# Optimization experiments

Measured on AMD Instinct MI355X. Metric: run time of the kernel, lower is better.

Reference implementation:

```python
import jax, jax.numpy as jnp
import numpy as np
import math

NH = 8      # n_heads
EPS = 1e-5  # LayerNorm eps (torch default)

def _pe(S, D):
    # Sin/cos positional encoding, faithful to PositionalEncoder
    pos = jnp.arange(S, dtype=jnp.float32)[:, None]
    div = jnp.exp(jnp.arange(0, D, 2, dtype=jnp.float32) * (-math.log(10000.0) / D))
    ang = pos * div  # (S, D/2)
    pe = jnp.zeros((S, D), jnp.float32)
    pe = pe.at[:, 0::2].set(jnp.sin(ang)).at[:, 1::2].set(jnp.cos(ang))
    return pe

def _ln(x, g, b):
    m = x.mean(-1, keepdims=True)
    v = ((x - m) ** 2).mean(-1, keepdims=True)
    return (x - m) / jnp.sqrt(v + EPS) * g + b

def setup_inputs() -> dict:
    key = jax.random.key(0)
    ks = jax.random.split(key, 6)
    S, H, W, D, dff = 512, 4, 4, 512, 2048
    x = jax.random.normal(ks[0], (S, H, W, D), jnp.float32)
    s = 1.0 / math.sqrt(D)
    Wq = jax.random.normal(ks[1], (D, D), jnp.float32) * s      # w_qs (used for q, k, v in sincos path)
    Wfc = jax.random.normal(ks[2], (D, D), jnp.float32) * s     # fc (no bias)
    W1 = jax.random.normal(ks[3], (dff, D), jnp.float32) * s    # ffn.w1
    b1 = jnp.zeros((dff,), jnp.float32)
    W2 = jax.random.normal(ks[4], (D, dff), jnp.float32) * (1.0 / math.sqrt(dff))  # ffn.w2
    b2 = jnp.zeros((D,), jnp.float32)
    g1 = jnp.ones((D,), jnp.float32); be1 = jnp.zeros((D,), jnp.float32)
    g2 = jnp.ones((D,), jnp.float32); be2 = jnp.zeros((D,), jnp.float32)
    return dict(x=x, Wq=Wq, Wfc=Wfc, W1=W1, b1=b1, W2=W2, b2=b2,
                g1=g1, be1=be1, g2=g2, be2=be2)

def reference(x, Wq, Wfc, W1, b1, W2, b2, g1, be1, g2, be2):
    S, H, Wd, D = x.shape
    depth = D // NH
    # sincos path: ALL of q,k,v use w_qs (source bug) and q==k==v since inputs are identical
    q = x @ Wq.T + _pe(S, D)[:, None, None, :]               # (S,H,W,D)
    # torch .view: raw memory reinterpretation (S,H,W,D) -> (H,W,S,NH,depth), then transpose(2,3)
    q5 = jnp.swapaxes(q.reshape(H, Wd, S, NH, depth), 2, 3)  # (H,W,NH,S,depth)
    k_t = jnp.swapaxes(q5, 3, 4)                             # (H,W,NH,depth,S)
    scale = 1.0 / math.sqrt(depth)
    # 'hwink,hwijm->hwinm': k and j are summed INDEPENDENTLY (rank-1 outer product of sums)
    bmm_qk = jnp.einsum('hwink,hwijm->hwinm', q5 * scale, k_t)   # (H,W,NH,S,S)
    qk = jax.nn.softmax(bmm_qk, axis=-1)
    qk = jnp.einsum('hwink,hwijm->hwinm', qk, k_t)               # second context pass
    attn_weights = jax.nn.softmax(qk, axis=-1)
    out = jnp.einsum('hwijk,hwikn->hwijn', attn_weights, q5)     # v == q5; (H,W,NH,S,depth)
    attn_out = out.reshape(S, H, Wd, NH * depth) @ Wfc.T         # raw reshape back, then fc
    o1 = _ln(x + attn_out, g1, be1)
    ffn = jax.nn.relu(o1 @ W1.T + b1) @ W2.T + b2
    return _ln(o1 + ffn, g2, be2)
```

## Files before the change

### kernel.cpp

```cpp
#include <hip/hip_runtime.h>
#include <hip/hip_bf16.h>
#include <math.h>


typedef short short8 __attribute__((ext_vector_type(8)));
typedef float f32x4 __attribute__((ext_vector_type(4)));

#define LN10K_OVER_256 0.03597789207803197f

__device__ __forceinline__ void gload16(const short* g, short* l) {
  __builtin_amdgcn_global_load_lds(
      (const __attribute__((address_space(1))) void*)g,
      (__attribute__((address_space(3))) void*)l, 16, 0, 0);
}

#define BAR() do { asm volatile("" ::: "memory"); \
                   __builtin_amdgcn_s_barrier();  \
                   asm volatile("" ::: "memory"); } while (0)

__device__ __forceinline__ short8 ldsfrag(const short* opbuf, int R, int fq) {
  int sr = R >> 1;
  int sp = (((R & 1) << 2) | fq) ^ (sr & 7);
  return *(const short8*)(opbuf + sr * 64 + sp * 8);
}

template<bool DOSTAGE, int WAITK>
__device__ __forceinline__ void tile_step(
    short* ldsb, int cur, int nx, int tt, int koff,
    const short* Ag0, const short* Ag1, const short* Bg0, const short* Bg1,
    int w, int fr, int fq, int wm, int wn, f32x4 (&acc)[8][4]) {
  const short* Abuf = ldsb + cur * 16384;
  const short* Bbuf = Abuf + 8192;
  short8 af[4], bfr[4];
#pragma unroll
  for (int m = 0; m < 4; ++m) af[m] = ldsfrag(Abuf, wm + m * 16 + fr, fq);
#pragma unroll
  for (int n = 0; n < 4; ++n) bfr[n] = ldsfrag(Bbuf, wn + n * 16 + fr, fq);
  if (DOSTAGE) {
    int kb = koff + (tt + 2) * 32;
    gload16(Ag0 + kb, ldsb + nx * 16384 + w * 512);
    gload16(Ag1 + kb, ldsb + nx * 16384 + 4096 + w * 512);
  }
  BAR();
  __builtin_amdgcn_s_setprio(1);
#pragma unroll
  for (int m = 0; m < 4; ++m)
#pragma unroll
    for (int n = 0; n < 4; ++n)
      acc[m][n] = __builtin_amdgcn_mfma_f32_16x16x32_bf16(af[m], bfr[n],
                                                          acc[m][n], 0, 0, 0);
  __builtin_amdgcn_s_setprio(0);
  BAR();
#pragma unroll
  for (int m = 0; m < 4; ++m) af[m] = ldsfrag(Abuf, wm + 64 + m * 16 + fr, fq);
  if (DOSTAGE) {
    int kb = koff + (tt + 2) * 32;
    gload16(Bg0 + kb, ldsb + nx * 16384 + 8192 + w * 512);
    gload16(Bg1 + kb, ldsb + nx * 16384 + 8192 + 4096 + w * 512);
  }
  BAR();
  __builtin_amdgcn_s_setprio(1);
#pragma unroll
  for (int m = 0; m < 4; ++m)
#pragma unroll
    for (int n = 0; n < 4; ++n)
      acc[4 + m][n] = __builtin_amdgcn_mfma_f32_16x16x32_bf16(af[m], bfr[n],
                                                              acc[4 + m][n], 0, 0, 0);
  __builtin_amdgcn_s_setprio(0);
  if (WAITK == 4) asm volatile("s_waitcnt vmcnt(4)" ::: "memory");
  else if (WAITK == 0) asm volatile("s_waitcnt vmcnt(0)" ::: "memory");
  BAR();
}

template<int MODE, int NT>
__global__ __launch_bounds__(512) void gemm256(
    const short* __restrict__ A, const short* __restrict__ B,
    const float* __restrict__ bias, short* __restrict__ C0,
    int ldC, int ldA, int ldB) {
  __shared__ short lds[3 * 2 * 8192];
  const int t = threadIdx.x;
  const int w = t >> 6, l = t & 63;
  const int fr = l & 15, fq = l >> 4;
  const int wm = (w >> 2) * 128;
  const int wn = (w & 3) * 64;
  const int m0 = blockIdx.y * 256, n0 = blockIdx.x * 256;
  const int koff = 0;

  const int scont = (t & 7) ^ ((t >> 3) & 7);
  const int Rbase = ((t >> 3) << 1) | (scont >> 2);
  const int cg = (scont & 3) << 3;
  const short* Ag0 = A + (size_t)(m0 + Rbase) * ldA + cg;
  const short* Ag1 = Ag0 + (size_t)128 * ldA;
  const short* Bg0 = B + (size_t)(n0 + Rbase) * ldB + cg;
  const short* Bg1 = Bg0 + (size_t)128 * ldB;
  short* ldsb = &lds[0];

  gload16(Ag0, ldsb + w * 512);
  gload16(Ag1, ldsb + 4096 + w * 512);
  gload16(Bg0, ldsb + 8192 + w * 512);
  gload16(Bg1, ldsb + 8192 + 4096 + w * 512);
  gload16(Ag0 + 32, ldsb + 16384 + w * 512);
  gload16(Ag1 + 32, ldsb + 16384 + 4096 + w * 512);
  gload16(Bg0 + 32, ldsb + 16384 + 8192 + w * 512);
  gload16(Bg1 + 32, ldsb + 16384 + 8192 + 4096 + w * 512);
  asm volatile("s_waitcnt vmcnt(4)" ::: "memory");
  BAR();

  f32x4 acc[8][4] = {};
  int cur = 0;
#pragma unroll 1
  for (int tt = 0; tt < NT - 2; ++tt) {
    int nx = cur + 2; if (nx >= 3) nx -= 3;
    tile_step<true, 4>(ldsb, cur, nx, tt, koff, Ag0, Ag1, Bg0, Bg1,
                       w, fr, fq, wm, wn, acc);
    if (++cur == 3) cur = 0;
  }
  tile_step<false, 0>(ldsb, cur, 0, NT - 2, koff, Ag0, Ag1, Bg0, Bg1,
                      w, fr, fq, wm, wn, acc);
  { int c2 = cur + 1; if (c2 >= 3) c2 -= 3;
    tile_step<false, -1>(ldsb, c2, 0, NT - 1, koff, Ag0, Ag1, Bg0, Bg1,
                         w, fr, fq, wm, wn, acc); }

  float bv[4];
#pragma unroll
  for (int n = 0; n < 4; ++n) bv[n] = bias[n0 + wn + n * 16 + fr];
#pragma unroll
  for (int mm = 0; mm < 8; ++mm) {
#pragma unroll
    for (int n = 0; n < 4; ++n) {
      int col = n0 + wn + n * 16 + fr;
#pragma unroll
      for (int j = 0; j < 4; ++j) {
        int row = m0 + wm + mm * 16 + fq * 4 + j;
        float v = fmaxf(acc[mm][n][j] + bv[n], 0.f);
        __hip_bfloat16 hb = __float2bfloat16(v);
        C0[(size_t)row * ldC + col] = *(short*)&hb;
      }
    }
  }
}

template<bool DOSTAGE, int WAITK>
__device__ __forceinline__ void tile_step128(
    short* ldsb, int cur, int nx, int tt,
    const short* Ag0, const short* Ag1, const short* Bg0, const short* Bg1,
    int w, int fr, int fq, int wm, int wn, f32x4 (&acc)[4][4]) {
  const short* Abuf = ldsb + cur * 8192;
  const short* Bbuf = Abuf + 4096;
  short8 af[4], bfr[4];
#pragma unroll
  for (int m = 0; m < 4; ++m) af[m] = ldsfrag(Abuf, wm + m * 16 + fr, fq);
#pragma unroll
  for (int n = 0; n < 4; ++n) bfr[n] = ldsfrag(Bbuf, wn + n * 16 + fr, fq);
  if (DOSTAGE) {
    int kb = (tt + 2) * 32;
    gload16(Ag0 + kb, ldsb + nx * 8192 + w * 512);
    gload16(Ag1 + kb, ldsb + nx * 8192 + 2048 + w * 512);
    gload16(Bg0 + kb, ldsb + nx * 8192 + 4096 + w * 512);
    gload16(Bg1 + kb, ldsb + nx * 8192 + 6144 + w * 512);
  }
  BAR();
  __builtin_amdgcn_s_setprio(1);
#pragma unroll
  for (int m = 0; m < 4; ++m)
#pragma unroll
    for (int n = 0; n < 4; ++n)
      acc[m][n] = __builtin_amdgcn_mfma_f32_16x16x32_bf16(af[m], bfr[n],
                                                          acc[m][n], 0, 0, 0);
  __builtin_amdgcn_s_setprio(0);
  if (WAITK == 4) asm volatile("s_waitcnt vmcnt(4)" ::: "memory");
  else if (WAITK == 0) asm volatile("s_waitcnt vmcnt(0)" ::: "memory");
  BAR();
}

template<int MODE, int NT>
__global__ __launch_bounds__(256) void gemm128(
    const short* __restrict__ A, const short* __restrict__ B,
    const float* __restrict__ bias, short* __restrict__ C,
    int ldC, int ldA, int ldB) {
  __shared__ short lds[3 * 8192];
  const int t = threadIdx.x;
  const int w = t >> 6, l = t & 63;
  const int fr = l & 15, fq = l >> 4;
  const int wm = (w >> 1) * 64;
  const int wn = (w & 1) * 64;
  const int m0 = blockIdx.y * 128, n0 = blockIdx.x * 128;

  const int scont = (t & 7) ^ ((t >> 3) & 7);
  const int Rbase = ((t >> 3) << 1) | (scont >> 2);
  const int cg = (scont & 3) << 3;
  const short* Ag0 = A + (size_t)(m0 + Rbase) * ldA + cg;
  const short* Ag1 = Ag0 + (size_t)64 * ldA;
  const short* Bg0 = B + (size_t)(n0 + Rbase) * ldB + cg;
  const short* Bg1 = Bg0 + (size_t)64 * ldB;
  short* ldsb = &lds[0];

  gload16(Ag0, ldsb + w * 512);
  gload16(Ag1, ldsb + 2048 + w * 512);
  gload16(Bg0, ldsb + 4096 + w * 512);
  gload16(Bg1, ldsb + 6144 + w * 512);
  gload16(Ag0 + 32, ldsb + 8192 + w * 512);
  gload16(Ag1 + 32, ldsb + 8192 + 2048 + w * 512);
  gload16(Bg0 + 32, ldsb + 8192 + 4096 + w * 512);
  gload16(Bg1 + 32, ldsb + 8192 + 6144 + w * 512);
  asm volatile("s_waitcnt vmcnt(4)" ::: "memory");
  BAR();

  f32x4 acc[4][4] = {};
  int cur = 0;
#pragma unroll 1
  for (int tt = 0; tt < NT - 2; ++tt) {
    int nx = cur + 2; if (nx >= 3) nx -= 3;
    tile_step128<true, 4>(ldsb, cur, nx, tt, Ag0, Ag1, Bg0, Bg1,
                          w, fr, fq, wm, wn, acc);
    if (++cur == 3) cur = 0;
  }
  tile_step128<false, 0>(ldsb, cur, 0, NT - 2, Ag0, Ag1, Bg0, Bg1,
                         w, fr, fq, wm, wn, acc);
  { int c2 = cur + 1; if (c2 >= 3) c2 -= 3;
    tile_step128<false, -1>(ldsb, c2, 0, NT - 1, Ag0, Ag1, Bg0, Bg1,
                            w, fr, fq, wm, wn, acc); }

  float bv[4];
  if (MODE == 2) {
#pragma unroll
    for (int n = 0; n < 4; ++n) bv[n] = bias[n0 + wn + n * 16 + fr];
  }
#pragma unroll
  for (int mm = 0; mm < 4; ++mm) {
    const float* per = nullptr;
    if (MODE == 0) {
      int s = (m0 + wm + mm * 16) >> 4;
      per = bias + (size_t)s * 512;
    }
#pragma unroll
    for (int n = 0; n < 4; ++n) {
      int col = n0 + wn + n * 16 + fr;
      float pv = (MODE == 0) ? per[col] : bv[n];
#pragma unroll
      for (int j = 0; j < 4; ++j) {
        int row = m0 + wm + mm * 16 + fq * 4 + j;
        float v = acc[mm][n][j] + pv;
        __hip_bfloat16 hb = __float2bfloat16(v);
        C[(size_t)row * ldC + col] = *(short*)&hb;
      }
    }
  }
}

__device__ __forceinline__ void cvt8(const float* in, short* out, int i) {
  const float4* p = (const float4*)(in + (size_t)i * 8);
  float4 a = p[0], b = p[1];
  union { __hip_bfloat16 h[8]; short8 s; } u;
  u.h[0] = __float2bfloat16(a.x); u.h[1] = __float2bfloat16(a.y);
  u.h[2] = __float2bfloat16(a.z); u.h[3] = __float2bfloat16(a.w);
  u.h[4] = __float2bfloat16(b.x); u.h[5] = __float2bfloat16(b.y);
  u.h[6] = __float2bfloat16(b.z); u.h[7] = __float2bfloat16(b.w);
  *(short8*)(out + (size_t)i * 8) = u.s;
}

__global__ __launch_bounds__(256) void prep(
    const float* __restrict__ x, const float* __restrict__ W1,
    const float* __restrict__ W2, const float* __restrict__ Wq,
    const float* __restrict__ Wfc,
    short* __restrict__ xb, short* __restrict__ W1b,
    short* __restrict__ W2b, short* __restrict__ Wqb,
    float* __restrict__ wsum, float* __restrict__ pe) {
  int b = blockIdx.x, t = threadIdx.x;
  if (b < 2048) {
    cvt8(x, xb, b * 256 + t);
  } else if (b < 2560) {
    cvt8(W1, W1b, (b - 2048) * 256 + t);
  } else if (b < 3072) {
    cvt8(W2, W2b, (b - 2560) * 256 + t);
  } else if (b < 3200) {
    cvt8(Wq, Wqb, (b - 3072) * 256 + t);
  } else if (b < 3328) {
    int idx = (b - 3200) * 256 + t;
    int n = idx >> 6, d = idx & 63;
    float s = 0.f;
#pragma unroll
    for (int j = 0; j < 8; ++j) s += Wfc[(size_t)n * 512 + j * 64 + d];
    wsum[idx] = s;
  } else {
    int idx = (b - 3328) * 256 + t;
    int s = idx >> 9, c = idx & 511;
    float f = expf(-(float)(c >> 1) * LN10K_OVER_256);
    float ang = (float)s * f;
    pe[idx] = (c & 1) ? cosf(ang) : sinf(ang);
  }
}

__global__ __launch_bounds__(256) void attn_g(
    const short* __restrict__ qb, const float* __restrict__ x,
    const float* __restrict__ wsum, const float* __restrict__ g1,
    const float* __restrict__ be1, float* __restrict__ o1,
    short* __restrict__ o1b) {
  int g = blockIdx.x;
  int hw = g >> 3, i = g & 7;
  int t = threadIdx.x;
  __shared__ short sl[512 * 72];
  __shared__ float a_[512];
  __shared__ float adist_[512];
  __shared__ float pctx[4][64];
  __shared__ float gb[1024];
  __shared__ float redA[4], redB[4], redMS[2];
  __shared__ float ctxs[64];

  gb[t] = g1[t]; gb[t + 256] = g1[t + 256];
  gb[512 + t] = be1[t]; gb[768 + t] = be1[t + 256];

  {
    const short* qsrc = qb + ((size_t)hw * 512) * 512 + i * 64;
    int chunk = t & 7, jr0 = t >> 3;
#pragma unroll
    for (int rep = 0; rep < 16; ++rep) {
      int j = jr0 + rep * 32;
      *(short8*)&sl[j * 72 + chunk * 8] =
          *(const short8*)(qsrc + (size_t)j * 512 + chunk * 8);
    }
  }
  __syncthreads();

  float r0 = 0.f, r1 = 0.f;
#pragma unroll
  for (int c = 0; c < 8; ++c) {
    union { short8 s8; short e[8]; } u0, u1;
    u0.s8 = *(const short8*)&sl[t * 72 + c * 8];
    u1.s8 = *(const short8*)&sl[(t + 256) * 72 + c * 8];
#pragma unroll
    for (int u = 0; u < 8; ++u) {
      r0 += __bfloat162float(*(__hip_bfloat16*)&u0.e[u]);
      r1 += __bfloat162float(*(__hip_bfloat16*)&u1.e[u]);
    }
  }
  float m = fmaxf(r0, r1);
  for (int off = 32; off; off >>= 1) m = fmaxf(m, __shfl_down(m, off));
  int wid = t >> 6, lane = t & 63;
  if (lane == 0) redA[wid] = m;
  __syncthreads();
  if (t == 0) redMS[0] = fmaxf(fmaxf(redA[0], redA[1]), fmaxf(redA[2], redA[3]));
  __syncthreads();
  float M = redMS[0];
  float e0 = expf(r0 - M), e1 = expf(r1 - M);
  float s = e0 + e1;
  for (int off = 32; off; off >>= 1) s += __shfl_down(s, off);
  if (lane == 0) redB[wid] = s;
  __syncthreads();
  if (t == 0) redMS[1] = redB[0] + redB[1] + redB[2] + redB[3];
  __syncthreads();
  float inv = 1.f / redMS[1];
  a_[t] = e0 * inv;
  a_[t + 256] = e1 * inv;
  __syncthreads();

  {
    int d = t & 63, seg = t >> 6;
    float acc = 0.f;
    for (int mm = seg * 128; mm < seg * 128 + 128; ++mm)
      acc += a_[mm] * __bfloat162float(*(__hip_bfloat16*)&sl[mm * 72 + d]);
    pctx[seg][d] = acc;
  }
  __syncthreads();
  if (t < 64) ctxs[t] = pctx[0][t] + pctx[1][t] + pctx[2][t] + pctx[3][t];
  __syncthreads();

  for (int n = t; n < 512; n += 256) {
    const float4* wr = (const float4*)(wsum + (size_t)n * 64);
    float sa = 0.f;
#pragma unroll
    for (int db = 0; db < 16; ++db) {
      float4 wv = wr[db];
      float4 cv = *(const float4*)&ctxs[db * 4];
      sa += cv.x * wv.x + cv.y * wv.y + cv.z * wv.z + cv.w * wv.w;
    }
    adist_[n] = sa;
  }
  __syncthreads();

  const float4* x4 = (const float4*)x;
  int w = t >> 6;
#pragma unroll 1
  for (int u = 0; u < 16; ++u) {
    int j = i * 64 + w * 16 + u;
    size_t R = (size_t)hw * 512 + j;
    float4 xv0 = x4[R * 128 + lane * 2];
    float4 xv1 = x4[R * 128 + lane * 2 + 1];
    float4 a0 = *(const float4*)&adist_[lane * 8];
    float4 a1 = *(const float4*)&adist_[lane * 8 + 4];
    float v[8] = {xv0.x + a0.x, xv0.y + a0.y, xv0.z + a0.z, xv0.w + a0.w,
                  xv1.x + a1.x, xv1.y + a1.y, xv1.z + a1.z, xv1.w + a1.w};
    float sm_ = 0.f, sq = 0.f;
#pragma unroll
    for (int q = 0; q < 8; ++q) { sm_ += v[q]; sq += v[q] * v[q]; }
    for (int off = 32; off; off >>= 1) {
      sm_ += __shfl_xor(sm_, off);
      sq += __shfl_xor(sq, off);
    }
    float mean = sm_ * (1.f / 512.f);
    float var = sq * (1.f / 512.f) - mean * mean;
    float rinv = rsqrtf(var + 1e-5f);
    float o[8];
    union { __hip_bfloat16 h[8]; short8 s8; } ub;
#pragma unroll
    for (int q = 0; q < 8; ++q) {
      int c = lane * 8 + q;
      o[q] = (v[q] - mean) * rinv * gb[c] + gb[512 + c];
      ub.h[q] = __float2bfloat16(o[q]);
    }
    float4 w0 = {o[0], o[1], o[2], o[3]};
    float4 w1 = {o[4], o[5], o[6], o[7]};
    *(float4*)&o1[R * 512 + lane * 8] = w0;
    *(float4*)&o1[R * 512 + lane * 8 + 4] = w1;
    *(short8*)&o1b[R * 512 + lane * 8] = ub.s8;
  }
}

__global__ __launch_bounds__(256) void ln2_fused(
    const float* __restrict__ o1, const short* __restrict__ f2,
    const float* __restrict__ gamma, const float* __restrict__ beta,
    float* __restrict__ Out) {
  int r = blockIdx.x;
  int t = threadIdx.x;
  size_t base = (size_t)r * 512;
  float v0 = o1[base + t] +
             __bfloat162float(*(const __hip_bfloat16*)&f2[base + t]);
  float v1 = o1[base + t + 256] +
             __bfloat162float(*(const __hip_bfloat16*)&f2[base + t + 256]);
  float s = v0 + v1, sq = v0 * v0 + v1 * v1;
  __shared__ float red[6];
  __shared__ float redA[4];
  __shared__ float redB[4];
  for (int off = 32; off; off >>= 1) {
    s += __shfl_down(s, off);
    sq += __shfl_down(sq, off);
  }
  int wid = t >> 6, lane = t & 63;
  if (lane == 0) { redA[wid] = s; redB[wid] = sq; }
  __syncthreads();
  if (t == 0) {
    float S = redA[0] + redA[1] + redA[2] + redA[3];
    float Q = redB[0] + redB[1] + redB[2] + redB[3];
    float mean = S * (1.f / 512.f);
    float var = Q * (1.f / 512.f) - mean * mean;
    red[4] = mean;
    red[5] = rsqrtf(var + 1e-5f);
  }
  __syncthreads();
  float mean = red[4], inv = red[5];
  Out[base + t] = (v0 - mean) * inv * gamma[t] + beta[t];
  Out[base + t + 256] = (v1 - mean) * inv * gamma[t + 256] + beta[t + 256];
}

extern "C" void kernel_launch(void* const* d_in, const int* in_sizes, int n_in,
                              void* d_out, int out_size, void* d_ws, size_t ws_size,
                              hipStream_t stream) {
  const float* x   = (const float*)d_in[0];
  const float* Wq  = (const float*)d_in[1];
  const float* Wfc = (const float*)d_in[2];
  const float* W1  = (const float*)d_in[3];
  const float* b1  = (const float*)d_in[4];
  const float* W2  = (const float*)d_in[5];
  const float* b2  = (const float*)d_in[6];
  const float* g1  = (const float*)d_in[7];
  const float* be1 = (const float*)d_in[8];
  const float* g2  = (const float*)d_in[9];
  const float* be2 = (const float*)d_in[10];
  float* out = (float*)d_out;

  char* ws = (char*)d_ws;
  float* o1   = (float*)(ws);
  short* h1b  = (short*)(ws + (16u << 20));
  short* f2b  = (short*)(ws + (48u << 20));
  short* o1b  = (short*)(ws + (56u << 20));
  short* W1b  = (short*)(ws + (64u << 20));
  short* W2b  = (short*)(ws + (66u << 20));
  short* Wqb  = (short*)(ws + (68u << 20));
  short* xb   = (short*)(ws + (69u << 20));
  short* qb   = (short*)(ws + (77u << 20));
  float* wsum = (float*)(ws + (85u << 20));
  float* pe   = (float*)(ws + (85u << 20) + (128u << 10));

  prep<<<4352, 256, 0, stream>>>(x, W1, W2, Wq, Wfc, xb, W1b, W2b, Wqb, wsum, pe);
  gemm128<0, 16><<<dim3(4, 64), 256, 0, stream>>>(
      xb, Wqb, pe, qb, 512, 512, 512);
  attn_g<<<128, 256, 0, stream>>>(qb, x, wsum, g1, be1, o1, o1b);
  gemm256<1, 16><<<dim3(8, 32), 512, 0, stream>>>(
      o1b, W1b, b1, h1b, 2048, 512, 512);
  gemm128<2, 64><<<dim3(4, 64), 256, 0, stream>>>(
      h1b, W2b, b2, f2b, 512, 2048, 2048);
  ln2_fused<<<8192, 256, 0, stream>>>(o1, f2b, g2, be2, out);
}
```

Baseline: 103.1 us.

## Split-K the Q projection and FFN down-projection GEMMs across two partial buffers

The 128-tile GEMMs for the Q projection and the FFN second layer now run with a grid z-dimension of 2, each half covering half of K and writing separate partial outputs. The Q partials are stored in fp32 and summed in attn_g while loading; the FFN partials are stored in bf16 and summed with the bias in ln2_fused. The aim is to double the block count from 256 to 512 so the GPU's compute units are better occupied. The cost is extra partial-buffer writes and reads. Storing FFN partials in bf16 adds one more rounding step before the sum.

```diff
diff --git a/kernel.cpp b/kernel.cpp
--- a/kernel.cpp
+++ b/kernel.cpp
@@ -26,7 +26,7 @@
 
 template<bool DOSTAGE, int WAITK>
 __device__ __forceinline__ void tile_step(
-    short* ldsb, int cur, int nx, int tt, int koff,
+    short* ldsb, int cur, int nx, int tt,
     const short* Ag0, const short* Ag1, const short* Bg0, const short* Bg1,
     int w, int fr, int fq, int wm, int wn, f32x4 (&acc)[8][4]) {
   const short* Abuf = ldsb + cur * 16384;
@@ -37,7 +37,7 @@
 #pragma unroll
   for (int n = 0; n < 4; ++n) bfr[n] = ldsfrag(Bbuf, wn + n * 16 + fr, fq);
   if (DOSTAGE) {
-    int kb = koff + (tt + 2) * 32;
+    int kb = (tt + 2) * 32;
     gload16(Ag0 + kb, ldsb + nx * 16384 + w * 512);
     gload16(Ag1 + kb, ldsb + nx * 16384 + 4096 + w * 512);
   }
@@ -54,7 +54,7 @@
 #pragma unroll
   for (int m = 0; m < 4; ++m) af[m] = ldsfrag(Abuf, wm + 64 + m * 16 + fr, fq);
   if (DOSTAGE) {
-    int kb = koff + (tt + 2) * 32;
+    int kb = (tt + 2) * 32;
     gload16(Bg0 + kb, ldsb + nx * 16384 + 8192 + w * 512);
     gload16(Bg1 + kb, ldsb + nx * 16384 + 8192 + 4096 + w * 512);
   }
@@ -84,7 +84,6 @@
   const int wm = (w >> 2) * 128;
   const int wn = (w & 3) * 64;
   const int m0 = blockIdx.y * 256, n0 = blockIdx.x * 256;
-  const int koff = 0;
 
   const int scont = (t & 7) ^ ((t >> 3) & 7);
   const int Rbase = ((t >> 3) << 1) | (scont >> 2);
@@ -111,14 +110,14 @@
 #pragma unroll 1
   for (int tt = 0; tt < NT - 2; ++tt) {
     int nx = cur + 2; if (nx >= 3) nx -= 3;
-    tile_step<true, 4>(ldsb, cur, nx, tt, koff, Ag0, Ag1, Bg0, Bg1,
+    tile_step<true, 4>(ldsb, cur, nx, tt, Ag0, Ag1, Bg0, Bg1,
                        w, fr, fq, wm, wn, acc);
     if (++cur == 3) cur = 0;
   }
-  tile_step<false, 0>(ldsb, cur, 0, NT - 2, koff, Ag0, Ag1, Bg0, Bg1,
+  tile_step<false, 0>(ldsb, cur, 0, NT - 2, Ag0, Ag1, Bg0, Bg1,
                       w, fr, fq, wm, wn, acc);
   { int c2 = cur + 1; if (c2 >= 3) c2 -= 3;
-    tile_step<false, -1>(ldsb, c2, 0, NT - 1, koff, Ag0, Ag1, Bg0, Bg1,
+    tile_step<false, -1>(ldsb, c2, 0, NT - 1, Ag0, Ag1, Bg0, Bg1,
                          w, fr, fq, wm, wn, acc); }
 
   float bv[4];
@@ -142,7 +141,7 @@
 
 template<bool DOSTAGE, int WAITK>
 __device__ __forceinline__ void tile_step128(
-    short* ldsb, int cur, int nx, int tt,
+    short* ldsb, int cur, int nx, int tt, int koff,
     const short* Ag0, const short* Ag1, const short* Bg0, const short* Bg1,
     int w, int fr, int fq, int wm, int wn, f32x4 (&acc)[4][4]) {
   const short* Abuf = ldsb + cur * 8192;
@@ -153,7 +152,7 @@
 #pragma unroll
   for (int n = 0; n < 4; ++n) bfr[n] = ldsfrag(Bbuf, wn + n * 16 + fr, fq);
   if (DOSTAGE) {
-    int kb = (tt + 2) * 32;
+    int kb = koff + (tt + 2) * 32;
     gload16(Ag0 + kb, ldsb + nx * 8192 + w * 512);
     gload16(Ag1 + kb, ldsb + nx * 8192 + 2048 + w * 512);
     gload16(Bg0 + kb, ldsb + nx * 8192 + 4096 + w * 512);
@@ -176,7 +175,9 @@
 template<int MODE, int NT>
 __global__ __launch_bounds__(256) void gemm128(
     const short* __restrict__ A, const short* __restrict__ B,
-    const float* __restrict__ bias, short* __restrict__ C,
+    const float* __restrict__ bias,
+    short* __restrict__ C0, short* __restrict__ C1,
+    float* __restrict__ F0, float* __restrict__ F1,
     int ldC, int ldA, int ldB) {
   __shared__ short lds[3 * 8192];
   const int t = threadIdx.x;
@@ -185,6 +186,8 @@
   const int wm = (w >> 1) * 64;
   const int wn = (w & 1) * 64;
   const int m0 = blockIdx.y * 128, n0 = blockIdx.x * 128;
+  const int z = blockIdx.z;
+  const int koff = z * (NT * 32);
 
   const int scont = (t & 7) ^ ((t >> 3) & 7);
   const int Rbase = ((t >> 3) << 1) | (scont >> 2);
@@ -195,14 +198,14 @@
   const short* Bg1 = Bg0 + (size_t)64 * ldB;
   short* ldsb = &lds[0];
 
-  gload16(Ag0, ldsb + w * 512);
-  gload16(Ag1, ldsb + 2048 + w * 512);
-  gload16(Bg0, ldsb + 4096 + w * 512);
-  gload16(Bg1, ldsb + 6144 + w * 512);
-  gload16(Ag0 + 32, ldsb + 8192 + w * 512);
-  gload16(Ag1 + 32, ldsb + 8192 + 2048 + w * 512);
-  gload16(Bg0 + 32, ldsb + 8192 + 4096 + w * 512);
-  gload16(Bg1 + 32, ldsb + 8192 + 6144 + w * 512);
+  gload16(Ag0 + koff, ldsb + w * 512);
+  gload16(Ag1 + koff, ldsb + 2048 + w * 512);
+  gload16(Bg0 + koff, ldsb + 4096 + w * 512);
+  gload16(Bg1 + koff, ldsb + 6144 + w * 512);
+  gload16(Ag0 + koff + 32, ldsb + 8192 + w * 512);
+  gload16(Ag1 + koff + 32, ldsb + 8192 + 2048 + w * 512);
+  gload16(Bg0 + koff + 32, ldsb + 8192 + 4096 + w * 512);
+  gload16(Bg1 + koff + 32, ldsb + 8192 + 6144 + w * 512);
   asm volatile("s_waitcnt vmcnt(4)" ::: "memory");
   BAR();
 
@@ -211,21 +214,16 @@
 #pragma unroll 1
   for (int tt = 0; tt < NT - 2; ++tt) {
     int nx = cur + 2; if (nx >= 3) nx -= 3;
-    tile_step128<true, 4>(ldsb, cur, nx, tt, Ag0, Ag1, Bg0, Bg1,
+    tile_step128<true, 4>(ldsb, cur, nx, tt, koff, Ag0, Ag1, Bg0, Bg1,
                           w, fr, fq, wm, wn, acc);
     if (++cur == 3) cur = 0;
   }
-  tile_step128<false, 0>(ldsb, cur, 0, NT - 2, Ag0, Ag1, Bg0, Bg1,
+  tile_step128<false, 0>(ldsb, cur, 0, NT - 2, koff, Ag0, Ag1, Bg0, Bg1,
                          w, fr, fq, wm, wn, acc);
   { int c2 = cur + 1; if (c2 >= 3) c2 -= 3;
-    tile_step128<false, -1>(ldsb, c2, 0, NT - 1, Ag0, Ag1, Bg0, Bg1,
+    tile_step128<false, -1>(ldsb, c2, 0, NT - 1, koff, Ag0, Ag1, Bg0, Bg1,
                             w, fr, fq, wm, wn, acc); }
 
-  float bv[4];
-  if (MODE == 2) {
-#pragma unroll
-    for (int n = 0; n < 4; ++n) bv[n] = bias[n0 + wn + n * 16 + fr];
-  }
 #pragma unroll
   for (int mm = 0; mm < 4; ++mm) {
     const float* per = nullptr;
@@ -236,13 +234,19 @@
 #pragma unroll
     for (int n = 0; n < 4; ++n) {
       int col = n0 + wn + n * 16 + fr;
-      float pv = (MODE == 0) ? per[col] : bv[n];
+      float pv = (MODE == 0 && z == 0) ? per[col] : 0.f;
 #pragma unroll
       for (int j = 0; j < 4; ++j) {
         int row = m0 + wm + mm * 16 + fq * 4 + j;
         float v = acc[mm][n][j] + pv;
-        __hip_bfloat16 hb = __float2bfloat16(v);
-        C[(size_t)row * ldC + col] = *(short*)&hb;
+        if (MODE == 0) {
+          float* myF = z ? F1 : F0;
+          myF[(size_t)row * ldC + col] = v;
+        } else {
+          short* myC = z ? C1 : C0;
+          __hip_bfloat16 hb = __float2bfloat16(v);
+          myC[(size_t)row * ldC + col] = *(short*)&hb;
+        }
       }
     }
   }
@@ -292,7 +296,8 @@
 }
 
 __global__ __launch_bounds__(256) void attn_g(
-    const short* __restrict__ qb, const float* __restrict__ x,
+    const float* __restrict__ qp0, const float* __restrict__ qp1,
+    const float* __restrict__ x,
     const float* __restrict__ wsum, const float* __restrict__ g1,
     const float* __restrict__ be1, float* __restrict__ o1,
     short* __restrict__ o1b) {
@@ -311,13 +316,28 @@
   gb[512 + t] = be1[t]; gb[768 + t] = be1[t + 256];
 
   {
-    const short* qsrc = qb + ((size_t)hw * 512) * 512 + i * 64;
+    size_t boff = ((size_t)hw * 512) * 512 + i * 64;
+    const float* q0 = qp0 + boff;
+    const float* q1 = qp1 + boff;
     int chunk = t & 7, jr0 = t >> 3;
 #pragma unroll
     for (int rep = 0; rep < 16; ++rep) {
       int j = jr0 + rep * 32;
-      *(short8*)&sl[j * 72 + chunk * 8] =
-          *(const short8*)(qsrc + (size_t)j * 512 + chunk * 8);
+      size_t off = (size_t)j * 512 + chunk * 8;
+      float4 a0 = *(const float4*)(q0 + off);
+      float4 a1 = *(const float4*)(q0 + off + 4);
+      float4 b0 = *(const float4*)(q1 + off);
+      float4 b1 = *(const float4*)(q1 + off + 4);
+      union { __hip_bfloat16 h[8]; short8 s8; } uo;
+      uo.h[0] = __float2bfloat16(a0.x + b0.x);
+      uo.h[1] = __float2bfloat16(a0.y + b0.y);
+      uo.h[2] = __float2bfloat16(a0.z + b0.z);
+      uo.h[3] = __float2bfloat16(a0.w + b0.w);
+      uo.h[4] = __float2bfloat16(a1.x + b1.x);
+      uo.h[5] = __float2bfloat16(a1.y + b1.y);
+      uo.h[6] = __float2bfloat16(a1.z + b1.z);
+      uo.h[7] = __float2bfloat16(a1.w + b1.w);
+      *(short8*)&sl[j * 72 + chunk * 8] = uo.s8;
     }
   }
   __syncthreads();
@@ -417,17 +437,23 @@
 }
 
 __global__ __launch_bounds__(256) void ln2_fused(
-    const float* __restrict__ o1, const short* __restrict__ f2,
-    const float* __restrict__ gamma, const float* __restrict__ beta,
-    float* __restrict__ Out) {
+    const float* __restrict__ o1,
+    const short* __restrict__ p0, const short* __restrict__ p1,
+    const float* __restrict__ b2, const float* __restrict__ gamma,
+    const float* __restrict__ beta, float* __restrict__ Out) {
   int r = blockIdx.x;
   int t = threadIdx.x;
   size_t base = (size_t)r * 512;
-  float v0 = o1[base + t] +
-             __bfloat162float(*(const __hip_bfloat16*)&f2[base + t]);
-  float v1 = o1[base + t + 256] +
-             __bfloat162float(*(const __hip_bfloat16*)&f2[base + t + 256]);
-  float s = v0 + v1, sq = v0 * v0 + v1 * v1;
+  float v[2];
+#pragma unroll
+  for (int h = 0; h < 2; ++h) {
+    int c = t + h * 256;
+    float f = b2[c];
+    f += __bfloat162float(*(const __hip_bfloat16*)&p0[base + c]);
+    f += __bfloat162float(*(const __hip_bfloat16*)&p1[base + c]);
+    v[h] = o1[base + c] + f;
+  }
+  float s = v[0] + v[1], sq = v[0] * v[0] + v[1] * v[1];
   __shared__ float red[6];
   __shared__ float redA[4];
   __shared__ float redB[4];
@@ -448,8 +474,8 @@
   }
   __syncthreads();
   float mean = red[4], inv = red[5];
-  Out[base + t] = (v0 - mean) * inv * gamma[t] + beta[t];
-  Out[base + t + 256] = (v1 - mean) * inv * gamma[t + 256] + beta[t + 256];
+  Out[base + t] = (v[0] - mean) * inv * gamma[t] + beta[t];
+  Out[base + t + 256] = (v[1] - mean) * inv * gamma[t + 256] + beta[t + 256];
 }
 
 extern "C" void kernel_launch(void* const* d_in, const int* in_sizes, int n_in,
@@ -469,25 +495,27 @@
   float* out = (float*)d_out;
 
   char* ws = (char*)d_ws;
-  float* o1   = (float*)(ws);
-  short* h1b  = (short*)(ws + (16u << 20));
-  short* f2b  = (short*)(ws + (48u << 20));
-  short* o1b  = (short*)(ws + (56u << 20));
-  short* W1b  = (short*)(ws + (64u << 20));
-  short* W2b  = (short*)(ws + (66u << 20));
-  short* Wqb  = (short*)(ws + (68u << 20));
-  short* xb   = (short*)(ws + (69u << 20));
-  short* qb   = (short*)(ws + (77u << 20));
-  float* wsum = (float*)(ws + (85u << 20));
-  float* pe   = (float*)(ws + (85u << 20) + (128u << 10));
+  float* o1    = (float*)(ws);
+  short* h1b   = (short*)(ws + (16u << 20));
+  short* pz0   = (short*)(ws + (48u << 20));
+  short* pz1   = (short*)(ws + (56u << 20));
+  short* o1b   = (short*)(ws + (64u << 20));
+  short* W1b   = (short*)(ws + (72u << 20));
+  short* W2b   = (short*)(ws + (74u << 20));
+  short* Wqb   = (short*)(ws + (76u << 20));
+  short* xb    = (short*)(ws + (77u << 20));
+  float* qp0f  = (float*)(ws + (85u << 20));
+  float* qp1f  = (float*)(ws + (101u << 20));
+  float* wsum  = (float*)(ws + (117u << 20));
+  float* pe    = (float*)(ws + (117u << 20) + (128u << 10));
 
   prep<<<4352, 256, 0, stream>>>(x, W1, W2, Wq, Wfc, xb, W1b, W2b, Wqb, wsum, pe);
-  gemm128<0, 16><<<dim3(4, 64), 256, 0, stream>>>(
-      xb, Wqb, pe, qb, 512, 512, 512);
-  attn_g<<<128, 256, 0, stream>>>(qb, x, wsum, g1, be1, o1, o1b);
+  gemm128<0, 8><<<dim3(4, 64, 2), 256, 0, stream>>>(
+      xb, Wqb, pe, nullptr, nullptr, qp0f, qp1f, 512, 512, 512);
+  attn_g<<<128, 256, 0, stream>>>(qp0f, qp1f, x, wsum, g1, be1, o1, o1b);
   gemm256<1, 16><<<dim3(8, 32), 512, 0, stream>>>(
       o1b, W1b, b1, h1b, 2048, 512, 512);
-  gemm128<2, 64><<<dim3(4, 64), 256, 0, stream>>>(
-      h1b, W2b, b2, f2b, 512, 2048, 2048);
-  ln2_fused<<<8192, 256, 0, stream>>>(o1, f2b, g2, be2, out);
-}
+  gemm128<3, 32><<<dim3(4, 64, 2), 256, 0, stream>>>(
+      h1b, W2b, nullptr, pz0, pz1, nullptr, nullptr, 512, 2048, 2048);
+  ln2_fused<<<8192, 256, 0, stream>>>(o1, pz0, pz1, b2, g2, be2, out);
+}
```

Measured after the change: 110.9 us. 7.6% more time.

## Fuse Q projection GEMM into attention kernel, computing q tiles in LDS

Applied to the files above, without the earlier changes.

The separate x·Wq^T GEMM and its bf16 q buffer are removed. Each attention block now computes its own 512x64 q slice with an MFMA pipeline over LDS, adds the positional encoding, and writes the result straight into the shared tile that the attention reduction reads. This saves a kernel launch and a global round trip for q. In exchange, the projection runs on only 128 blocks instead of 256, and each block has a large LDS footprint that limits occupancy.

```diff
diff --git a/kernel.cpp b/kernel.cpp
--- a/kernel.cpp
+++ b/kernel.cpp
@@ -26,7 +26,7 @@
 
 template<bool DOSTAGE, int WAITK>
 __device__ __forceinline__ void tile_step(
-    short* ldsb, int cur, int nx, int tt, int koff,
+    short* ldsb, int cur, int nx, int tt,
     const short* Ag0, const short* Ag1, const short* Bg0, const short* Bg1,
     int w, int fr, int fq, int wm, int wn, f32x4 (&acc)[8][4]) {
   const short* Abuf = ldsb + cur * 16384;
@@ -37,7 +37,7 @@
 #pragma unroll
   for (int n = 0; n < 4; ++n) bfr[n] = ldsfrag(Bbuf, wn + n * 16 + fr, fq);
   if (DOSTAGE) {
-    int kb = koff + (tt + 2) * 32;
+    int kb = (tt + 2) * 32;
     gload16(Ag0 + kb, ldsb + nx * 16384 + w * 512);
     gload16(Ag1 + kb, ldsb + nx * 16384 + 4096 + w * 512);
   }
@@ -54,7 +54,7 @@
 #pragma unroll
   for (int m = 0; m < 4; ++m) af[m] = ldsfrag(Abuf, wm + 64 + m * 16 + fr, fq);
   if (DOSTAGE) {
-    int kb = koff + (tt + 2) * 32;
+    int kb = (tt + 2) * 32;
     gload16(Bg0 + kb, ldsb + nx * 16384 + 8192 + w * 512);
     gload16(Bg1 + kb, ldsb + nx * 16384 + 8192 + 4096 + w * 512);
   }
@@ -72,7 +72,7 @@
   BAR();
 }
 
-template<int MODE, int NT>
+template<int NT>
 __global__ __launch_bounds__(512) void gemm256(
     const short* __restrict__ A, const short* __restrict__ B,
     const float* __restrict__ bias, short* __restrict__ C0,
@@ -84,7 +84,6 @@
   const int wm = (w >> 2) * 128;
   const int wn = (w & 3) * 64;
   const int m0 = blockIdx.y * 256, n0 = blockIdx.x * 256;
-  const int koff = 0;
 
   const int scont = (t & 7) ^ ((t >> 3) & 7);
   const int Rbase = ((t >> 3) << 1) | (scont >> 2);
@@ -111,14 +110,14 @@
 #pragma unroll 1
   for (int tt = 0; tt < NT - 2; ++tt) {
     int nx = cur + 2; if (nx >= 3) nx -= 3;
-    tile_step<true, 4>(ldsb, cur, nx, tt, koff, Ag0, Ag1, Bg0, Bg1,
+    tile_step<true, 4>(ldsb, cur, nx, tt, Ag0, Ag1, Bg0, Bg1,
                        w, fr, fq, wm, wn, acc);
     if (++cur == 3) cur = 0;
   }
-  tile_step<false, 0>(ldsb, cur, 0, NT - 2, koff, Ag0, Ag1, Bg0, Bg1,
+  tile_step<false, 0>(ldsb, cur, 0, NT - 2, Ag0, Ag1, Bg0, Bg1,
                       w, fr, fq, wm, wn, acc);
   { int c2 = cur + 1; if (c2 >= 3) c2 -= 3;
-    tile_step<false, -1>(ldsb, c2, 0, NT - 1, koff, Ag0, Ag1, Bg0, Bg1,
+    tile_step<false, -1>(ldsb, c2, 0, NT - 1, Ag0, Ag1, Bg0, Bg1,
                          w, fr, fq, wm, wn, acc); }
 
   float bv[4];
@@ -173,7 +172,7 @@
   BAR();
 }
 
-template<int MODE, int NT>
+template<int NT>
 __global__ __launch_bounds__(256) void gemm128(
     const short* __restrict__ A, const short* __restrict__ B,
     const float* __restrict__ bias, short* __restrict__ C,
@@ -222,25 +221,17 @@
                             w, fr, fq, wm, wn, acc); }
 
   float bv[4];
-  if (MODE == 2) {
-#pragma unroll
-    for (int n = 0; n < 4; ++n) bv[n] = bias[n0 + wn + n * 16 + fr];
-  }
+#pragma unroll
+  for (int n = 0; n < 4; ++n) bv[n] = bias[n0 + wn + n * 16 + fr];
 #pragma unroll
   for (int mm = 0; mm < 4; ++mm) {
-    const float* per = nullptr;
-    if (MODE == 0) {
-      int s = (m0 + wm + mm * 16) >> 4;
-      per = bias + (size_t)s * 512;
-    }
 #pragma unroll
     for (int n = 0; n < 4; ++n) {
       int col = n0 + wn + n * 16 + fr;
-      float pv = (MODE == 0) ? per[col] : bv[n];
 #pragma unroll
       for (int j = 0; j < 4; ++j) {
         int row = m0 + wm + mm * 16 + fq * 4 + j;
-        float v = acc[mm][n][j] + pv;
+        float v = acc[mm][n][j] + bv[n];
         __hip_bfloat16 hb = __float2bfloat16(v);
         C[(size_t)row * ldC + col] = *(short*)&hb;
       }
@@ -291,33 +282,113 @@
   }
 }
 
+template<bool DOSTAGE, int WAITK>
+__device__ __forceinline__ void tile_step_attn(
+    short* lds0, int cur, int nx, int tt,
+    const short* Ag, const short* Bg,
+    int w, int fr, int fq, int wm, f32x4 (&acc)[8][4]) {
+  const short* Abuf = lds0 + cur * 18432;
+  const short* Bbuf = Abuf + 16384;
+  short8 af[8], bfr[4];
+#pragma unroll
+  for (int m = 0; m < 8; ++m) af[m] = ldsfrag(Abuf, wm + m * 16 + fr, fq);
+#pragma unroll
+  for (int n = 0; n < 4; ++n) bfr[n] = ldsfrag(Bbuf, n * 16 + fr, fq);
+  if (DOSTAGE) {
+    int kb = (tt + 2) * 32;
+    short* dst = lds0 + nx * 18432;
+#pragma unroll
+    for (int k = 0; k < 8; ++k)
+      gload16(Ag + kb + (size_t)(k * 64) * 512, dst + k * 2048 + w * 512);
+    gload16(Bg + kb, dst + 16384 + w * 512);
+  }
+  BAR();
+  __builtin_amdgcn_s_setprio(1);
+#pragma unroll
+  for (int m = 0; m < 8; ++m)
+#pragma unroll
+    for (int n = 0; n < 4; ++n)
+      acc[m][n] = __builtin_amdgcn_mfma_f32_16x16x32_bf16(af[m], bfr[n],
+                                                          acc[m][n], 0, 0, 0);
+  __builtin_amdgcn_s_setprio(0);
+  if (WAITK == 9) asm volatile("s_waitcnt vmcnt(9)" ::: "memory");
+  else if (WAITK == 0) asm volatile("s_waitcnt vmcnt(0)" ::: "memory");
+  BAR();
+}
+
 __global__ __launch_bounds__(256) void attn_g(
-    const short* __restrict__ qb, const float* __restrict__ x,
+    const short* __restrict__ xb, const short* __restrict__ Wqb,
+    const float* __restrict__ pe, const float* __restrict__ x,
     const float* __restrict__ wsum, const float* __restrict__ g1,
     const float* __restrict__ be1, float* __restrict__ o1,
     short* __restrict__ o1b) {
   int g = blockIdx.x;
   int hw = g >> 3, i = g & 7;
   int t = threadIdx.x;
-  __shared__ short sl[512 * 72];
+  __shared__ short ldsbuf[3 * 18432];
   __shared__ float a_[512];
   __shared__ float adist_[512];
   __shared__ float pctx[4][64];
   __shared__ float gb[1024];
   __shared__ float redA[4], redB[4], redMS[2];
   __shared__ float ctxs[64];
+  short* sl = ldsbuf;
+
+  const int w = t >> 6, l = t & 63;
+  const int fr = l & 15, fq = l >> 4;
+  const int wm = w * 128;
+  const int lane = l;
 
   gb[t] = g1[t]; gb[t + 256] = g1[t + 256];
   gb[512 + t] = be1[t]; gb[768 + t] = be1[t + 256];
 
-  {
-    const short* qsrc = qb + ((size_t)hw * 512) * 512 + i * 64;
-    int chunk = t & 7, jr0 = t >> 3;
-#pragma unroll
-    for (int rep = 0; rep < 16; ++rep) {
-      int j = jr0 + rep * 32;
-      *(short8*)&sl[j * 72 + chunk * 8] =
-          *(const short8*)(qsrc + (size_t)j * 512 + chunk * 8);
+  const int scont = (t & 7) ^ ((t >> 3) & 7);
+  const int Rbase = ((t >> 3) << 1) | (scont >> 2);
+  const int cg = (scont & 3) << 3;
+  const short* Ag = xb + ((size_t)hw * 512 + Rbase) * 512 + cg;
+  const short* Bg = Wqb + ((size_t)i * 64 + Rbase) * 512 + cg;
+
+#pragma unroll
+  for (int tb = 0; tb < 2; ++tb) {
+    short* dst = ldsbuf + tb * 18432;
+    int kb = tb * 32;
+#pragma unroll
+    for (int k = 0; k < 8; ++k)
+      gload16(Ag + kb + (size_t)(k * 64) * 512, dst + k * 2048 + w * 512);
+    gload16(Bg + kb, dst + 16384 + w * 512);
+  }
+  asm volatile("s_waitcnt vmcnt(9)" ::: "memory");
+  BAR();
+
+  f32x4 acc[8][4] = {};
+  int cur = 0;
+#pragma unroll 1
+  for (int tt = 0; tt < 14; ++tt) {
+    int nx = cur + 2; if (nx >= 3) nx -= 3;
+    tile_step_attn<true, 9>(ldsbuf, cur, nx, tt, Ag, Bg, w, fr, fq, wm, acc);
+    if (++cur == 3) cur = 0;
+  }
+  tile_step_attn<false, 0>(ldsbuf, cur, 0, 14, Ag, Bg, w, fr, fq, wm, acc);
+  { int c2 = cur + 1; if (c2 >= 3) c2 -= 3;
+    tile_step_attn<false, -1>(ldsbuf, c2, 0, 15, Ag, Bg, w, fr, fq, wm, acc); }
+
+  asm volatile("s_waitcnt lgkmcnt(0)" ::: "memory");
+  BAR();
+
+#pragma unroll
+  for (int m = 0; m < 8; ++m) {
+    int rbase = wm + m * 16;
+    const float* per = pe + ((size_t)(hw * 32 + (rbase >> 4))) * 512 + i * 64;
+#pragma unroll
+    for (int n = 0; n < 4; ++n) {
+      int col = n * 16 + fr;
+      float pv = per[col];
+#pragma unroll
+      for (int jj = 0; jj < 4; ++jj) {
+        int row = rbase + fq * 4 + jj;
+        __hip_bfloat16 hb = __float2bfloat16(acc[m][n][jj] + pv);
+        sl[row * 72 + col] = *(short*)&hb;
+      }
     }
   }
   __syncthreads();
@@ -336,7 +407,7 @@
   }
   float m = fmaxf(r0, r1);
   for (int off = 32; off; off >>= 1) m = fmaxf(m, __shfl_down(m, off));
-  int wid = t >> 6, lane = t & 63;
+  int wid = t >> 6;
   if (lane == 0) redA[wid] = m;
   __syncthreads();
   if (t == 0) redMS[0] = fmaxf(fmaxf(redA[0], redA[1]), fmaxf(redA[2], redA[3]));
@@ -356,10 +427,10 @@
 
   {
     int d = t & 63, seg = t >> 6;
-    float acc = 0.f;
+    float acc2 = 0.f;
     for (int mm = seg * 128; mm < seg * 128 + 128; ++mm)
-      acc += a_[mm] * __bfloat162float(*(__hip_bfloat16*)&sl[mm * 72 + d]);
-    pctx[seg][d] = acc;
+      acc2 += a_[mm] * __bfloat162float(*(__hip_bfloat16*)&sl[mm * 72 + d]);
+    pctx[seg][d] = acc2;
   }
   __syncthreads();
   if (t < 64) ctxs[t] = pctx[0][t] + pctx[1][t] + pctx[2][t] + pctx[3][t];
@@ -379,7 +450,6 @@
   __syncthreads();
 
   const float4* x4 = (const float4*)x;
-  int w = t >> 6;
 #pragma unroll 1
   for (int u = 0; u < 16; ++u) {
     int j = i * 64 + w * 16 + u;
@@ -477,17 +547,14 @@
   short* W2b  = (short*)(ws + (66u << 20));
   short* Wqb  = (short*)(ws + (68u << 20));
   short* xb   = (short*)(ws + (69u << 20));
-  short* qb   = (short*)(ws + (77u << 20));
-  float* wsum = (float*)(ws + (85u << 20));
-  float* pe   = (float*)(ws + (85u << 20) + (128u << 10));
+  float* wsum = (float*)(ws + (77u << 20));
+  float* pe   = (float*)(ws + (77u << 20) + (128u << 10));
 
   prep<<<4352, 256, 0, stream>>>(x, W1, W2, Wq, Wfc, xb, W1b, W2b, Wqb, wsum, pe);
-  gemm128<0, 16><<<dim3(4, 64), 256, 0, stream>>>(
-      xb, Wqb, pe, qb, 512, 512, 512);
-  attn_g<<<128, 256, 0, stream>>>(qb, x, wsum, g1, be1, o1, o1b);
-  gemm256<1, 16><<<dim3(8, 32), 512, 0, stream>>>(
+  attn_g<<<128, 256, 0, stream>>>(xb, Wqb, pe, x, wsum, g1, be1, o1, o1b);
+  gemm256<16><<<dim3(8, 32), 512, 0, stream>>>(
       o1b, W1b, b1, h1b, 2048, 512, 512);
-  gemm128<2, 64><<<dim3(4, 64), 256, 0, stream>>>(
+  gemm128<64><<<dim3(4, 64), 256, 0, stream>>>(
       h1b, W2b, b2, f2b, 512, 2048, 2048);
   ln2_fused<<<8192, 256, 0, stream>>>(o1, f2b, g2, be2, out);
 }
```

Measured after the change: 110.5 us. 1.07x slower.
